# Performance work log

Measured on AMD Instinct MI355X. Metric: run time of the kernel, lower is better.

The kernel has to match this reference:

```python
import jax, jax.numpy as jnp
import numpy as np

NUM_HEADS = 8
GROUPS = 32
EPS = 1e-5


def group_norm(x, gamma, beta):
    # x: (b, c, L)
    b, c, L = x.shape
    xg = x.reshape(b, GROUPS, c // GROUPS, L)
    mean = xg.mean(axis=(2, 3), keepdims=True)
    var = xg.var(axis=(2, 3), keepdims=True)
    xn = ((xg - mean) / jnp.sqrt(var + EPS)).reshape(b, c, L)
    return xn * gamma[None, :, None] + beta[None, :, None]


def setup_inputs() -> dict:
    key = jax.random.key(0)
    ks = jax.random.split(key, 8)
    b, c, h, w = 8, 512, 32, 32
    inner = c  # inner_channels == -1 -> channels
    x = jax.random.normal(ks[0], (b, c, h, w), dtype=jnp.float32)
    gamma = jnp.ones((c,), dtype=jnp.float32)
    beta = jnp.zeros((c,), dtype=jnp.float32)
    Wq = jax.random.normal(ks[1], (inner, c), dtype=jnp.float32) * 0.02
    bq = jnp.zeros((inner,), dtype=jnp.float32)
    Wkv = jax.random.normal(ks[2], (2 * inner, c), dtype=jnp.float32) * 0.02
    bkv = jnp.zeros((2 * inner,), dtype=jnp.float32)
    Wo = jax.random.normal(ks[3], (c, inner), dtype=jnp.float32) * 0.02
    bo = jnp.zeros((c,), dtype=jnp.float32)
    return {"x": x, "gamma": gamma, "beta": beta, "Wq": Wq, "bq": bq,
            "Wkv": Wkv, "bkv": bkv, "Wo": Wo, "bo": bo}


def reference(x, gamma, beta, Wq, bq, Wkv, bkv, Wo, bo):
    b, c = x.shape[:2]
    spatial = x.shape[2:]
    L = int(np.prod(spatial))
    inner = Wq.shape[0]
    dh = inner // NUM_HEADS
    scale = dh ** -0.5  # NOTE: applied to BOTH q and k, as in the source

    xr = x.reshape(b, c, L)
    hn = group_norm(xr, gamma, beta)          # norm(x); also serves as context

    # 1x1 Conv1d == channel matmul
    q = jnp.einsum('oc,bcl->bol', Wq, hn) + bq[None, :, None]
    kv = jnp.einsum('oc,bcl->bol', Wkv, hn) + bkv[None, :, None]
    k, v = jnp.split(kv, 2, axis=1)

    # (b, heads, dh, L)
    qh = (q * scale).reshape(b, NUM_HEADS, dh, L)
    kh = (k * scale).reshape(b, NUM_HEADS, dh, L)
    vh = v.reshape(b, NUM_HEADS, dh, L)

    dots = jnp.einsum('bhdt,bhds->bhts', qh, kh)
    attn = jax.nn.softmax(dots.astype(jnp.float32), axis=-1).astype(dots.dtype)
    out = jnp.einsum('bhts,bhds->bhdt', attn, vh)  # (b, heads, dh, L)

    out = out.reshape(b, inner, L)
    # output Linear over the channel dim
    out = jnp.einsum('oc,bcl->bol', Wo, out) + bo[None, :, None]
    return (xr + out).reshape(b, c, *spatial)
```

## Files before the change

### kernel.cpp

```cpp
#include <hip/hip_runtime.h>
#include <math.h>

#define B_ 8
#define C_ 512
#define L_ 1024
#define NH_ 8
#define DH_ 64
#define EPS 1e-5f
#define SCALE 0.125f
#define QSCALE (0.125f * 1.44269504088896f)

typedef __bf16 bf16x8 __attribute__((ext_vector_type(8)));
typedef __bf16 bf16x4 __attribute__((ext_vector_type(4)));
typedef float  f32x4  __attribute__((ext_vector_type(4)));

#define MFMA16(a, b, c) __builtin_amdgcn_mfma_f32_16x16x32_bf16((a), (b), (c), 0, 0, 0)

__device__ __forceinline__ void glds16(const __bf16* g, __bf16* l) {
    __builtin_amdgcn_global_load_lds((const __attribute__((address_space(1))) void*)(g),
                                     (__attribute__((address_space(3))) void*)(l),
                                     16, 0, 0);
}

__global__ __launch_bounds__(256)
void prep_kernel(const float* __restrict__ Wq, const float* __restrict__ Wkv,
                 const float* __restrict__ Wo, __bf16* __restrict__ dst,
                 const float* __restrict__ x, float* __restrict__ stats) {
    __shared__ float rs[256], rss[256];
    int bid = blockIdx.x, tid = threadIdx.x;
    if (bid < 1024) {
        int idx = bid * 256 + tid;
        float4 v;
        if (idx < 65536)        v = ((const float4*)Wq)[idx];
        else if (idx < 196608)  v = ((const float4*)Wkv)[idx - 65536];
        else                    v = ((const float4*)Wo)[idx - 196608];
        bf16x4 o;
        o[0] = (__bf16)v.x; o[1] = (__bf16)v.y; o[2] = (__bf16)v.z; o[3] = (__bf16)v.w;
        ((bf16x4*)dst)[idx] = o;
        return;
    }
    int bg = bid - 1024;
    size_t goff = (size_t)bg * 16 * L_;
    const float4* x4 = (const float4*)(x + goff);
    float s = 0.f, ss = 0.f;
    for (int i = tid; i < 4096; i += 256) {
        float4 v = x4[i];
        s  += v.x + v.y + v.z + v.w;
        ss += v.x * v.x + v.y * v.y + v.z * v.z + v.w * v.w;
    }
    rs[tid] = s; rss[tid] = ss;
    __syncthreads();
    for (int off = 128; off > 0; off >>= 1) {
        if (tid < off) { rs[tid] += rs[tid + off]; rss[tid] += rss[tid + off]; }
        __syncthreads();
    }
    if (tid == 0) {
        const float inv_n = 1.f / 16384.f;
        float mean = rs[0] * inv_n;
        float var  = rss[0] * inv_n - mean * mean;
        stats[bg * 2]     = mean;
        stats[bg * 2 + 1] = rsqrtf(var + EPS);
    }
}

__global__ __launch_bounds__(256)
void gn_apply_kernel(const float* __restrict__ x, const float* __restrict__ gamma,
                     const float* __restrict__ beta, const float* __restrict__ stats,
                     __bf16* __restrict__ hnT) {
    __shared__ __bf16 T[32 * 520];
    const int lt = blockIdx.x, b = blockIdx.y;
    const int tid = threadIdx.x;
    const int l0 = lt * 32;
    const int cbase = tid >> 3, fl = tid & 7;
#pragma unroll
    for (int p = 0; p < 16; ++p) {
        int cc = cbase + p * 32;
        float4 v = *(const float4*)&x[((size_t)b * C_ + cc) * L_ + l0 + fl * 4];
        int bg = b * 32 + (cc >> 4);
        float m = stats[bg * 2], rstd = stats[bg * 2 + 1];
        float ga = gamma[cc] * rstd, be = beta[cc];
        T[(fl * 4 + 0) * 520 + cc] = (__bf16)((v.x - m) * ga + be);
        T[(fl * 4 + 1) * 520 + cc] = (__bf16)((v.y - m) * ga + be);
        T[(fl * 4 + 2) * 520 + cc] = (__bf16)((v.z - m) * ga + be);
        T[(fl * 4 + 3) * 520 + cc] = (__bf16)((v.w - m) * ga + be);
    }
    __syncthreads();
    const int lrow = tid >> 6, cu = tid & 63;
#pragma unroll
    for (int pp = 0; pp < 8; ++pp) {
        int l = pp * 4 + lrow;
        bf16x8 r = *(const bf16x8*)&T[l * 520 + cu * 8];
        *(bf16x8*)&hnT[((size_t)b * L_ + l0 + l) * C_ + cu * 8] = r;
    }
}

__device__ __forceinline__
void gemm_mainloop(const __bf16* __restrict__ A, const __bf16* __restrict__ Bp,
                   __bf16* As, __bf16* Bs, f32x4 acc[4][4]) {
    const int tid = threadIdx.x;
    const int lane = tid & 63, w = tid >> 6;
    const int c = lane & 15, q = lane >> 4;
    const int wm = (w >> 1) * 64, wn = (w & 1) * 64;
    const int l8 = lane >> 3, kgsw = (lane & 7) ^ l8;

    for (int k0 = 0; k0 < 512; k0 += 64) {
#pragma unroll
        for (int i = 0; i < 4; ++i) {
            int chunk = w * 4 + i;
            int row = chunk * 8 + l8;
            glds16(A  + (size_t)row * 512 + k0 + kgsw * 8, &As[chunk * 512]);
            glds16(Bp + (size_t)row * 512 + k0 + kgsw * 8, &Bs[chunk * 512]);
        }
        __syncthreads();
#pragma unroll
        for (int ks = 0; ks < 2; ++ks) {
            const int koff = ((ks * 4 + q) ^ (c & 7)) * 8;
            bf16x8 af[4], bfr[4];
#pragma unroll
            for (int m = 0; m < 4; ++m)
                af[m] = *(const bf16x8*)&As[(wm + m * 16 + c) * 64 + koff];
#pragma unroll
            for (int n = 0; n < 4; ++n)
                bfr[n] = *(const bf16x8*)&Bs[(wn + n * 16 + c) * 64 + koff];
#pragma unroll
            for (int m = 0; m < 4; ++m)
#pragma unroll
                for (int n = 0; n < 4; ++n)
                    acc[m][n] = MFMA16(af[m], bfr[n], acc[m][n]);
        }
        __syncthreads();
    }
}

__global__ __launch_bounds__(256)
void qkv_kernel(const __bf16* __restrict__ Wq_bf, const __bf16* __restrict__ Wkv_bf,
                const __bf16* __restrict__ hnT,
                const float* __restrict__ bq, const float* __restrict__ bkv,
                __bf16* __restrict__ qT, __bf16* __restrict__ kT,
                __bf16* __restrict__ vv) {
    __shared__ __bf16 SMEM[128 * 64 * 2];
    __bf16* As = SMEM;
    __bf16* Bs = SMEM + 128 * 64;
    const int b = blockIdx.y;
    const int xx = blockIdx.x;
    const int sec = xx >> 5, t = xx & 31;
    const __bf16* hb = hnT + (size_t)b * L_ * C_;

    const __bf16 *A, *Bp;
    int m0, n0;
    if (sec < 2) {
        m0 = (t & 3) * 128; n0 = (t >> 2) * 128;
        A  = (sec == 0 ? Wq_bf : Wkv_bf) + (size_t)m0 * 512;
        Bp = hb + (size_t)n0 * 512;
    } else {
        m0 = (t >> 2) * 128; n0 = (t & 3) * 128;
        A  = hb + (size_t)m0 * 512;
        Bp = Wkv_bf + (size_t)(512 + n0) * 512;
    }

    f32x4 acc[4][4];
#pragma unroll
    for (int m = 0; m < 4; ++m)
#pragma unroll
        for (int n = 0; n < 4; ++n)
#pragma unroll
            for (int r = 0; r < 4; ++r) acc[m][n][r] = 0.f;

    gemm_mainloop(A, Bp, As, Bs, acc);

    const int tid = threadIdx.x, lane = tid & 63, w = tid >> 6;
    const int c = lane & 15, q = lane >> 4;
    const int wm = (w >> 1) * 64, wn = (w & 1) * 64;

    __bf16* T2 = SMEM;
    const float* bias = (sec == 0) ? bq : bkv;
    const float scl = (sec == 0) ? QSCALE : SCALE;
#pragma unroll
    for (int mt = 0; mt < 4; ++mt)
#pragma unroll
        for (int nt = 0; nt < 4; ++nt) {
            int n_loc = wn + nt * 16 + c;
            int u4 = (wm >> 2) + mt * 4 + q;
            int u4sw = u4 ^ ((n_loc & 7) << 1);
            bf16x4 ov;
            if (sec < 2) {
                int ob = m0 + wm + mt * 16 + q * 4;
#pragma unroll
                for (int r = 0; r < 4; ++r)
                    ov[r] = (__bf16)((acc[mt][nt][r] + bias[ob + r]) * scl);
            } else {
                float bi = bkv[512 + n0 + n_loc];
#pragma unroll
                for (int r = 0; r < 4; ++r)
                    ov[r] = (__bf16)(acc[mt][nt][r] + bi);
            }
            *(bf16x4*)&T2[n_loc * 128 + u4sw * 4] = ov;
        }
    __syncthreads();
#pragma unroll
    for (int p = 0; p < 8; ++p) {
        int rrow = p * 16 + (tid >> 4);
        int u16 = tid & 15;
        int u4p = (u16 * 2) ^ ((rrow & 7) << 1);
        bf16x8 val = *(const bf16x8*)&T2[rrow * 128 + u4p * 4];
        if (sec < 2) {
            int l = n0 + rrow;
            int og = m0 + u16 * 8;
            int hh = og >> 6, d0 = og & 63;
            __bf16* dstp = (sec == 0) ? qT : kT;
            *(bf16x8*)&dstp[((size_t)(b * NH_ + hh) * L_ + l) * DH_ + d0] = val;
        } else {
            int o = n0 + rrow;
            int lg = m0 + u16 * 8;
            *(bf16x8*)&vv[((size_t)b * C_ + o) * L_ + lg] = val;
        }
    }
}

__global__ __launch_bounds__(512)
void attn_kernel(const __bf16* __restrict__ qT, const __bf16* __restrict__ kT,
                 const __bf16* __restrict__ vv, __bf16* __restrict__ aoT) {
    const int tt = blockIdx.x, h = blockIdx.y, b = blockIdx.z;
    const int t0 = tt * 128;
    __shared__ __bf16 Qs[128 * 64];
    __shared__ __bf16 Ks[2][64 * 64];
    __shared__ __bf16 Vs[2][64 * 64];
    __shared__ __bf16 Ones[16 * 64];
    __shared__ __bf16 Ps[128 * 72];

    const int tid = threadIdx.x, lane = tid & 63, w = tid >> 6;
    const int c = lane & 15, q = lane >> 4;
    const int l8 = lane >> 3, kg = (lane & 7) ^ l8;

    const __bf16* qbase = qT + ((size_t)(b * NH_ + h) * L_ + t0) * DH_;
    const __bf16* kbase = kT + (size_t)(b * NH_ + h) * L_ * DH_;
    const __bf16* vbase = vv + (size_t)(b * C_ + h * DH_) * L_;

    if (tid < 256) {
        int row = tid >> 4, u8 = tid & 15;
        int u8sw = (((u8 >> 1) ^ (row & 7)) << 1) | (u8 & 1);
        float fv = (row == 0) ? 1.f : 0.f;
        bf16x4 val;
        val[0] = (__bf16)fv; val[1] = (__bf16)fv; val[2] = (__bf16)fv; val[3] = (__bf16)fv;
        *(bf16x4*)&Ones[row * 64 + u8sw * 4] = val;
    }
#pragma unroll
    for (int i = 0; i < 2; ++i) {
        int chunk = w * 2 + i;
        int row = chunk * 8 + l8;
        glds16(qbase + (size_t)row * DH_ + kg * 8, &Qs[chunk * 512]);
    }
    {
        int row = w * 8 + l8;
        glds16(kbase + (size_t)row * DH_ + kg * 8, &Ks[0][w * 512]);
        glds16(vbase + (size_t)row * L_ + kg * 8, &Vs[0][w * 512]);
        glds16(kbase + (size_t)(64 + row) * DH_ + kg * 8, &Ks[1][w * 512]);
        glds16(vbase + (size_t)row * L_ + 64 + kg * 8, &Vs[1][w * 512]);
    }
    asm volatile("s_waitcnt vmcnt(2) lgkmcnt(0)" ::: "memory");
    asm volatile("s_barrier" ::: "memory");

    f32x4 o_acc[4], o_l;
#pragma unroll
    for (int dt = 0; dt < 4; ++dt)
#pragma unroll
        for (int r = 0; r < 4; ++r) o_acc[dt][r] = 0.f;
#pragma unroll
    for (int r = 0; r < 4; ++r) o_l[r] = 0.f;

    for (int it = 0; it < 16; ++it) {
        const __bf16* Kc = Ks[it & 1];
        const __bf16* Vc = Vs[it & 1];

        f32x4 sres[4];
#pragma unroll
        for (int mt = 0; mt < 4; ++mt)
#pragma unroll
            for (int r = 0; r < 4; ++r) sres[mt][r] = 0.f;
#pragma unroll
        for (int ks = 0; ks < 2; ++ks) {
            const int koff = ((ks * 4 + q) ^ (c & 7)) * 8;
            bf16x8 bQ = *(const bf16x8*)&Qs[(w * 16 + c) * 64 + koff];
#pragma unroll
            for (int mt = 0; mt < 4; ++mt) {
                bf16x8 aK = *(const bf16x8*)&Kc[(mt * 16 + c) * 64 + koff];
                sres[mt] = MFMA16(aK, bQ, sres[mt]);
            }
        }

        {
            int trow = w * 16 + c;
#pragma unroll
            for (int mt = 0; mt < 4; ++mt) {
                bf16x4 pv;
#pragma unroll
                for (int r = 0; r < 4; ++r) pv[r] = (__bf16)exp2f(sres[mt][r]);
                *(bf16x4*)&Ps[trow * 72 + (mt * 4 + q) * 4] = pv;
            }
        }

#pragma unroll
        for (int ks = 0; ks < 2; ++ks) {
            const int koff = ((ks * 4 + q) ^ (c & 7)) * 8;
            bf16x8 bp = *(const bf16x8*)&Ps[(w * 16 + c) * 72 + ks * 32 + q * 8];
            bf16x8 aO = *(const bf16x8*)&Ones[c * 64 + koff];
#pragma unroll
            for (int dt = 0; dt < 4; ++dt) {
                bf16x8 aV = *(const bf16x8*)&Vc[(dt * 16 + c) * 64 + koff];
                o_acc[dt] = MFMA16(aV, bp, o_acc[dt]);
            }
            o_l = MFMA16(aO, bp, o_l);
        }

        asm volatile("s_barrier" ::: "memory");
        if (it < 14) {
            int s0n = (it + 2) * 64;
            int row = w * 8 + l8;
            glds16(kbase + (size_t)(s0n + row) * DH_ + kg * 8, &Ks[it & 1][w * 512]);
            glds16(vbase + (size_t)row * L_ + s0n + kg * 8, &Vs[it & 1][w * 512]);
            asm volatile("s_waitcnt vmcnt(2)" ::: "memory");
        } else {
            asm volatile("s_waitcnt vmcnt(0)" ::: "memory");
        }
        asm volatile("s_barrier" ::: "memory");
    }

    {
        float lsum = __shfl(o_l[0], c);
        float linv = 1.f / lsum;
        int tg = t0 + w * 16 + c;
        __bf16* aobase = aoT + ((size_t)b * L_ + tg) * C_ + h * DH_;
#pragma unroll
        for (int dt = 0; dt < 4; ++dt) {
            bf16x4 ov;
#pragma unroll
            for (int r = 0; r < 4; ++r) ov[r] = (__bf16)(o_acc[dt][r] * linv);
            *(bf16x4*)&aobase[dt * 16 + q * 4] = ov;
        }
    }
}

__global__ __launch_bounds__(256)
void proj_kernel(const __bf16* __restrict__ aoT, const __bf16* __restrict__ Wo_bf,
                 const float* __restrict__ bo, const float* __restrict__ x,
                 float* __restrict__ out) {
    __shared__ __bf16 As[128 * 64], Bs[128 * 64];
    const int b = blockIdx.y, t = blockIdx.x;
    const int m0 = (t >> 2) * 128;
    const int n0 = (t & 3) * 128;
    const __bf16* A  = aoT + (size_t)b * L_ * C_ + (size_t)m0 * 512;
    const __bf16* Bp = Wo_bf + (size_t)n0 * 512;

    f32x4 acc[4][4];
#pragma unroll
    for (int m = 0; m < 4; ++m)
#pragma unroll
        for (int n = 0; n < 4; ++n)
#pragma unroll
            for (int r = 0; r < 4; ++r) acc[m][n][r] = 0.f;

    gemm_mainloop(A, Bp, As, Bs, acc);

    const int tid = threadIdx.x, lane = tid & 63, w = tid >> 6;
    const int c = lane & 15, q = lane >> 4;
    const int wm = (w >> 1) * 64, wn = (w & 1) * 64;

#pragma unroll
    for (int mt = 0; mt < 4; ++mt)
#pragma unroll
        for (int nt = 0; nt < 4; ++nt) {
            int lb = m0 + wm + mt * 16 + q * 4;
            int o  = n0 + wn + nt * 16 + c;
            float bi = bo[o];
            size_t off = ((size_t)b * C_ + o) * L_ + lb;
            float4 xv = *(const float4*)&x[off];
            float4 rv;
            rv.x = acc[mt][nt][0] + bi + xv.x;
            rv.y = acc[mt][nt][1] + bi + xv.y;
            rv.z = acc[mt][nt][2] + bi + xv.z;
            rv.w = acc[mt][nt][3] + bi + xv.w;
            *(float4*)&out[off] = rv;
        }
}

extern "C" void kernel_launch(void* const* d_in, const int* in_sizes, int n_in,
                              void* d_out, int out_size, void* d_ws, size_t ws_size,
                              hipStream_t stream) {
    const float* x     = (const float*)d_in[0];
    const float* gamma = (const float*)d_in[1];
    const float* beta  = (const float*)d_in[2];
    const float* Wq    = (const float*)d_in[3];
    const float* bq    = (const float*)d_in[4];
    const float* Wkv   = (const float*)d_in[5];
    const float* bkv   = (const float*)d_in[6];
    const float* Wo    = (const float*)d_in[7];
    const float* bo    = (const float*)d_in[8];
    float* out = (float*)d_out;

    __bf16* wsb = (__bf16*)d_ws;
    __bf16* Wq_bf  = wsb;
    __bf16* Wkv_bf = wsb + 262144;
    __bf16* Wo_bf  = wsb + 786432;
    __bf16* hnT    = wsb + 1048576;
    __bf16* qT     = wsb + 5242880;
    __bf16* kT     = wsb + 9437184;
    __bf16* vv     = wsb + 13631488;
    __bf16* aoT    = wsb + 17825792;
    float*  stats  = (float*)(wsb + 22020096);

    prep_kernel<<<dim3(1280), 256, 0, stream>>>(Wq, Wkv, Wo, wsb, x, stats);
    gn_apply_kernel<<<dim3(32, B_), 256, 0, stream>>>(x, gamma, beta, stats, hnT);
    qkv_kernel<<<dim3(96, B_), 256, 0, stream>>>(Wq_bf, Wkv_bf, hnT, bq, bkv, qT, kT, vv);
    attn_kernel<<<dim3(8, NH_, B_), 512, 0, stream>>>(qT, kT, vv, aoT);
    proj_kernel<<<dim3(32, B_), 256, 0, stream>>>(aoT, Wo_bf, bo, x, out);
}
```

Baseline: 169.5 us.

## Rewrite attention with 32x32 MFMA, register-resident P, and XCD-aware block mapping

Replaces the 16x16x32 MFMA attention inner loop with 32x32x16 MFMA tiles on 4 waves of 32 query rows each. The softmax probabilities are converted to bf16 and rearranged in registers with v_cvt_pk_bf16_f32 and v_permlane32_swap, so the LDS round-trip through Ps goes away. The row sum is computed in registers instead of with an extra MFMA against a ones matrix. The launch becomes a 1D grid with a block-index swizzle (likely to group K/V sharing across XCDs) and 256-thread blocks with two blocks per CU, which trades wave count per block for more accumulator registers per wave.

```diff
diff --git a/kernel.cpp b/kernel.cpp
--- a/kernel.cpp
+++ b/kernel.cpp
@@ -13,8 +13,10 @@
 typedef __bf16 bf16x8 __attribute__((ext_vector_type(8)));
 typedef __bf16 bf16x4 __attribute__((ext_vector_type(4)));
 typedef float  f32x4  __attribute__((ext_vector_type(4)));
+typedef float  f32x16 __attribute__((ext_vector_type(16)));
 
 #define MFMA16(a, b, c) __builtin_amdgcn_mfma_f32_16x16x32_bf16((a), (b), (c), 0, 0, 0)
+#define MFMA32(a, b, c) __builtin_amdgcn_mfma_f32_32x32x16_bf16((a), (b), (c), 0, 0, 0)
 
 __device__ __forceinline__ void glds16(const __bf16* g, __bf16* l) {
     __builtin_amdgcn_global_load_lds((const __attribute__((address_space(1))) void*)(g),
@@ -217,127 +219,133 @@
     }
 }
 
-__global__ __launch_bounds__(512)
+__global__ __launch_bounds__(256, 2)
 void attn_kernel(const __bf16* __restrict__ qT, const __bf16* __restrict__ kT,
                  const __bf16* __restrict__ vv, __bf16* __restrict__ aoT) {
-    const int tt = blockIdx.x, h = blockIdx.y, b = blockIdx.z;
+    const int bid = blockIdx.x;
+    const int wg = (bid & 7) * 64 + (bid >> 3);
+    const int tt = wg & 7, h = (wg >> 3) & 7, b = wg >> 6;
     const int t0 = tt * 128;
     __shared__ __bf16 Qs[128 * 64];
     __shared__ __bf16 Ks[2][64 * 64];
     __shared__ __bf16 Vs[2][64 * 64];
-    __shared__ __bf16 Ones[16 * 64];
-    __shared__ __bf16 Ps[128 * 72];
 
     const int tid = threadIdx.x, lane = tid & 63, w = tid >> 6;
-    const int c = lane & 15, q = lane >> 4;
     const int l8 = lane >> 3, kg = (lane & 7) ^ l8;
+    const int ln = lane & 31, hi = lane >> 5, r7 = ln & 7;
 
     const __bf16* qbase = qT + ((size_t)(b * NH_ + h) * L_ + t0) * DH_;
     const __bf16* kbase = kT + (size_t)(b * NH_ + h) * L_ * DH_;
     const __bf16* vbase = vv + (size_t)(b * C_ + h * DH_) * L_;
 
-    if (tid < 256) {
-        int row = tid >> 4, u8 = tid & 15;
-        int u8sw = (((u8 >> 1) ^ (row & 7)) << 1) | (u8 & 1);
-        float fv = (row == 0) ? 1.f : 0.f;
-        bf16x4 val;
-        val[0] = (__bf16)fv; val[1] = (__bf16)fv; val[2] = (__bf16)fv; val[3] = (__bf16)fv;
-        *(bf16x4*)&Ones[row * 64 + u8sw * 4] = val;
-    }
-#pragma unroll
-    for (int i = 0; i < 2; ++i) {
-        int chunk = w * 2 + i;
-        int row = chunk * 8 + l8;
-        glds16(qbase + (size_t)row * DH_ + kg * 8, &Qs[chunk * 512]);
-    }
-    {
-        int row = w * 8 + l8;
-        glds16(kbase + (size_t)row * DH_ + kg * 8, &Ks[0][w * 512]);
-        glds16(vbase + (size_t)row * L_ + kg * 8, &Vs[0][w * 512]);
-        glds16(kbase + (size_t)(64 + row) * DH_ + kg * 8, &Ks[1][w * 512]);
-        glds16(vbase + (size_t)row * L_ + 64 + kg * 8, &Vs[1][w * 512]);
-    }
-    asm volatile("s_waitcnt vmcnt(2) lgkmcnt(0)" ::: "memory");
+#pragma unroll
+    for (int i = 0; i < 4; ++i) {
+        int chunk = w * 4 + i;
+        glds16(qbase + (size_t)(chunk * 8 + l8) * DH_ + kg * 8, &Qs[chunk * 512]);
+    }
+#pragma unroll
+    for (int buf = 0; buf < 2; ++buf)
+#pragma unroll
+        for (int i = 0; i < 2; ++i) {
+            int chunk = w * 2 + i, row = chunk * 8 + l8;
+            glds16(kbase + (size_t)(buf * 64 + row) * DH_ + kg * 8, &Ks[buf][chunk * 512]);
+            glds16(vbase + (size_t)row * L_ + buf * 64 + kg * 8, &Vs[buf][chunk * 512]);
+        }
+    asm volatile("s_waitcnt vmcnt(4)" ::: "memory");
     asm volatile("s_barrier" ::: "memory");
 
-    f32x4 o_acc[4], o_l;
-#pragma unroll
-    for (int dt = 0; dt < 4; ++dt)
-#pragma unroll
-        for (int r = 0; r < 4; ++r) o_acc[dt][r] = 0.f;
-#pragma unroll
-    for (int r = 0; r < 4; ++r) o_l[r] = 0.f;
+    f32x16 o_acc[2];
+#pragma unroll
+    for (int dt = 0; dt < 2; ++dt)
+#pragma unroll
+        for (int r = 0; r < 16; ++r) o_acc[dt][r] = 0.f;
+    float l_own = 0.f;
+
+    const int qrow = w * 32 + ln;
 
     for (int it = 0; it < 16; ++it) {
         const __bf16* Kc = Ks[it & 1];
         const __bf16* Vc = Vs[it & 1];
 
-        f32x4 sres[4];
-#pragma unroll
-        for (int mt = 0; mt < 4; ++mt)
-#pragma unroll
-            for (int r = 0; r < 4; ++r) sres[mt][r] = 0.f;
-#pragma unroll
-        for (int ks = 0; ks < 2; ++ks) {
-            const int koff = ((ks * 4 + q) ^ (c & 7)) * 8;
-            bf16x8 bQ = *(const bf16x8*)&Qs[(w * 16 + c) * 64 + koff];
-#pragma unroll
-            for (int mt = 0; mt < 4; ++mt) {
-                bf16x8 aK = *(const bf16x8*)&Kc[(mt * 16 + c) * 64 + koff];
-                sres[mt] = MFMA16(aK, bQ, sres[mt]);
+        f32x16 sres[2];
+#pragma unroll
+        for (int mt = 0; mt < 2; ++mt)
+#pragma unroll
+            for (int r = 0; r < 16; ++r) sres[mt][r] = 0.f;
+#pragma unroll
+        for (int ks = 0; ks < 4; ++ks) {
+            bf16x8 bQ = *(const bf16x8*)&Qs[qrow * 64 + ((ks * 2 + hi) ^ r7) * 8];
+#pragma unroll
+            for (int mt = 0; mt < 2; ++mt) {
+                bf16x8 aK = *(const bf16x8*)&Kc[(mt * 32 + ln) * 64 + ((ks * 2 + hi) ^ r7) * 8];
+                sres[mt] = MFMA32(aK, bQ, sres[mt]);
             }
         }
 
-        {
-            int trow = w * 16 + c;
-#pragma unroll
-            for (int mt = 0; mt < 4; ++mt) {
-                bf16x4 pv;
-#pragma unroll
-                for (int r = 0; r < 4; ++r) pv[r] = (__bf16)exp2f(sres[mt][r]);
-                *(bf16x4*)&Ps[trow * 72 + (mt * 4 + q) * 4] = pv;
+        bf16x8 frag[4];
+#pragma unroll
+        for (int mt = 0; mt < 2; ++mt) {
+            float pv[16];
+#pragma unroll
+            for (int r = 0; r < 16; ++r) pv[r] = exp2f(sres[mt][r]);
+            float s0a = (pv[0] + pv[1]) + (pv[2] + pv[3]);
+            float s1a = (pv[4] + pv[5]) + (pv[6] + pv[7]);
+            float s2a = (pv[8] + pv[9]) + (pv[10] + pv[11]);
+            float s3a = (pv[12] + pv[13]) + (pv[14] + pv[15]);
+            l_own += (s0a + s1a) + (s2a + s3a);
+            unsigned int P[8];
+#pragma unroll
+            for (int j = 0; j < 8; ++j)
+                asm("v_cvt_pk_bf16_f32 %0, %1, %2" : "=v"(P[j]) : "v"(pv[2 * j]), "v"(pv[2 * j + 1]));
+            asm("v_permlane32_swap_b32 %0, %1" : "+v"(P[0]), "+v"(P[2]));
+            asm("v_permlane32_swap_b32 %0, %1" : "+v"(P[1]), "+v"(P[3]));
+            asm("v_permlane32_swap_b32 %0, %1" : "+v"(P[4]), "+v"(P[6]));
+            asm("v_permlane32_swap_b32 %0, %1" : "+v"(P[5]), "+v"(P[7]));
+            union FU { unsigned int u[4]; bf16x8 v; } fa, fb;
+            fa.u[0] = P[0]; fa.u[1] = P[1]; fa.u[2] = P[2]; fa.u[3] = P[3];
+            fb.u[0] = P[4]; fb.u[1] = P[5]; fb.u[2] = P[6]; fb.u[3] = P[7];
+            frag[mt * 2 + 0] = fa.v;
+            frag[mt * 2 + 1] = fb.v;
+        }
+
+#pragma unroll
+        for (int ks2 = 0; ks2 < 4; ++ks2) {
+#pragma unroll
+            for (int dt = 0; dt < 2; ++dt) {
+                bf16x8 aV = *(const bf16x8*)&Vc[(dt * 32 + ln) * 64 + ((ks2 * 2 + hi) ^ r7) * 8];
+                o_acc[dt] = MFMA32(aV, frag[ks2], o_acc[dt]);
             }
-        }
-
-#pragma unroll
-        for (int ks = 0; ks < 2; ++ks) {
-            const int koff = ((ks * 4 + q) ^ (c & 7)) * 8;
-            bf16x8 bp = *(const bf16x8*)&Ps[(w * 16 + c) * 72 + ks * 32 + q * 8];
-            bf16x8 aO = *(const bf16x8*)&Ones[c * 64 + koff];
-#pragma unroll
-            for (int dt = 0; dt < 4; ++dt) {
-                bf16x8 aV = *(const bf16x8*)&Vc[(dt * 16 + c) * 64 + koff];
-                o_acc[dt] = MFMA16(aV, bp, o_acc[dt]);
-            }
-            o_l = MFMA16(aO, bp, o_l);
         }
 
         asm volatile("s_barrier" ::: "memory");
         if (it < 14) {
             int s0n = (it + 2) * 64;
-            int row = w * 8 + l8;
-            glds16(kbase + (size_t)(s0n + row) * DH_ + kg * 8, &Ks[it & 1][w * 512]);
-            glds16(vbase + (size_t)row * L_ + s0n + kg * 8, &Vs[it & 1][w * 512]);
-            asm volatile("s_waitcnt vmcnt(2)" ::: "memory");
+#pragma unroll
+            for (int i = 0; i < 2; ++i) {
+                int chunk = w * 2 + i, row = chunk * 8 + l8;
+                glds16(kbase + (size_t)(s0n + row) * DH_ + kg * 8, &Ks[it & 1][chunk * 512]);
+                glds16(vbase + (size_t)row * L_ + s0n + kg * 8, &Vs[it & 1][chunk * 512]);
+            }
+            asm volatile("s_waitcnt vmcnt(4)" ::: "memory");
         } else {
             asm volatile("s_waitcnt vmcnt(0)" ::: "memory");
         }
         asm volatile("s_barrier" ::: "memory");
     }
 
-    {
-        float lsum = __shfl(o_l[0], c);
-        float linv = 1.f / lsum;
-        int tg = t0 + w * 16 + c;
-        __bf16* aobase = aoT + ((size_t)b * L_ + tg) * C_ + h * DH_;
-#pragma unroll
-        for (int dt = 0; dt < 4; ++dt) {
+    float l_tot = l_own + __shfl_xor(l_own, 32);
+    float linv = 1.f / l_tot;
+    const int tg = t0 + w * 32 + ln;
+    __bf16* aobase = aoT + ((size_t)b * L_ + tg) * C_ + h * DH_;
+#pragma unroll
+    for (int dt = 0; dt < 2; ++dt)
+#pragma unroll
+        for (int rq = 0; rq < 4; ++rq) {
             bf16x4 ov;
 #pragma unroll
-            for (int r = 0; r < 4; ++r) ov[r] = (__bf16)(o_acc[dt][r] * linv);
-            *(bf16x4*)&aobase[dt * 16 + q * 4] = ov;
-        }
-    }
+            for (int j = 0; j < 4; ++j) ov[j] = (__bf16)(o_acc[dt][rq * 4 + j] * linv);
+            *(bf16x4*)&aobase[dt * 32 + rq * 8 + hi * 4] = ov;
+        }
 }
 
 __global__ __launch_bounds__(256)
@@ -411,6 +419,6 @@
     prep_kernel<<<dim3(1280), 256, 0, stream>>>(Wq, Wkv, Wo, wsb, x, stats);
     gn_apply_kernel<<<dim3(32, B_), 256, 0, stream>>>(x, gamma, beta, stats, hnT);
     qkv_kernel<<<dim3(96, B_), 256, 0, stream>>>(Wq_bf, Wkv_bf, hnT, bq, bkv, qT, kT, vv);
-    attn_kernel<<<dim3(8, NH_, B_), 512, 0, stream>>>(qT, kT, vv, aoT);
+    attn_kernel<<<dim3(512), 256, 0, stream>>>(qT, kT, vv, aoT);
     proj_kernel<<<dim3(32, B_), 256, 0, stream>>>(aoT, Wo_bf, bo, x, out);
 }
```

Result: no change. 166.5 us (-1.8%).
